# Kernel optimization log

Hardware: AMD Instinct MI355X
Metric: run time of the kernel (lower is better)

## Reference

```python
import jax, jax.numpy as jnp
import numpy as np

B, C, P = 16, 512, 4096


def setup_inputs() -> dict:
    key = jax.random.key(0)
    ks = jax.random.split(key, 7)
    s = 1.0 / np.sqrt(C)  # torch Conv1d default init scale
    return {
        "x": jax.random.normal(ks[0], (B, C, P), dtype=jnp.float32),
        "Wq": jax.random.uniform(ks[1], (C, C), jnp.float32, -s, s),
        "bq": jax.random.uniform(ks[2], (C,), jnp.float32, -s, s),
        "Wk": jax.random.uniform(ks[3], (C, C), jnp.float32, -s, s),
        "bk": jax.random.uniform(ks[4], (C,), jnp.float32, -s, s),
        "Wv": jax.random.uniform(ks[5], (C, C), jnp.float32, -s, s),
        "bv": jax.random.uniform(ks[6], (C,), jnp.float32, -s, s),
    }


def reference(x, Wq, bq, Wk, bk, Wv, bv):
    # 1x1 Conv1d == channel-mixing GEMM: out[b,o,p] = sum_i W[o,i] x[b,i,p] + b[o]
    q = jnp.einsum('oi,bip->bop', Wq, x) + bq[None, :, None]   # [B,C,P]
    k = jnp.einsum('oi,bip->bop', Wk, x) + bk[None, :, None]   # [B,C,P]
    v = jnp.einsum('oi,bip->bop', Wv, x) + bv[None, :, None]   # [B,C,P]
    energy = jnp.einsum('bcp,bdp->bcd', q, k)                  # [B,C,C] (unscaled)
    attn = jax.nn.softmax(energy, axis=-1)
    out = jnp.einsum('bcd,bdp->bcp', attn, v)                  # [B,C,P]
    return out
```

## Files before the change

### kernel.cpp

```cpp
#include <hip/hip_runtime.h>
#include <hip/hip_bf16.h>

#define CD 512
#define PD 4096
#define BD 16
#define CAUG 640
#define KW 576
#define GKS 4

typedef __bf16 bf16x8 __attribute__((ext_vector_type(8)));
typedef float f32x4 __attribute__((ext_vector_type(4)));
typedef unsigned short u16x8 __attribute__((ext_vector_type(8)));
typedef unsigned short u16x4 __attribute__((ext_vector_type(4)));

__device__ __forceinline__ unsigned short f2bf(float f) {
  unsigned u = __builtin_bit_cast(unsigned, f);
  u += 0x7FFFu + ((u >> 16) & 1u);
  return (unsigned short)(u >> 16);
}
__device__ __forceinline__ float bf2f(unsigned short h) {
  unsigned u = ((unsigned)h) << 16;
  return __builtin_bit_cast(float, u);
}

__global__ void convert_w2(const float* __restrict__ Wq, const float* __restrict__ bq,
                           const float* __restrict__ Wk, const float* __restrict__ bk,
                           const float* __restrict__ Wv,
                           unsigned short* __restrict__ Wqh, unsigned short* __restrict__ Wql,
                           unsigned short* __restrict__ Wkh, unsigned short* __restrict__ Wkl,
                           unsigned short* __restrict__ Wvh) {
  int i = blockIdx.x * 256 + threadIdx.x;
  if (i >= CD * KW) return;
  int o = i / KW, j = i - o * KW;
  float q = j < CD ? Wq[o * CD + j] : (j == CD ? bq[o] : 0.f);
  float k = j < CD ? Wk[o * CD + j] : (j == CD ? bk[o] : 0.f);
  unsigned short qh = f2bf(q), kh = f2bf(k);
  Wqh[i] = qh; Wql[i] = f2bf(q - bf2f(qh));
  Wkh[i] = kh; Wkl[i] = f2bf(k - bf2f(kh));
  if (j < CD) Wvh[o * CD + j] = f2bf(Wv[o * CD + j]);
}

__global__ void convert_x(const float* __restrict__ x, unsigned short* __restrict__ xsh,
                          unsigned short* __restrict__ xsl, unsigned short* __restrict__ xth) {
  int z = blockIdx.z, cy = blockIdx.y;
  int p0 = blockIdx.x * 64;
  int t = threadIdx.x;
  if (cy >= 8) {
    int row = 512 + (cy - 8) * 64 + (t >> 2);
    int cg = (t & 3) * 16;
    u16x8 h = (u16x8)0, l = (u16x8)0;
    if (row == 512)
#pragma unroll
      for (int i = 0; i < 8; ++i) h[i] = 0x3F80;
    size_t o = (size_t)z * CAUG * PD + (size_t)row * PD + p0 + cg;
    *reinterpret_cast<u16x8*>(xsh + o) = h;
    *reinterpret_cast<u16x8*>(xsh + o + 8) = h;
    *reinterpret_cast<u16x8*>(xsl + o) = l;
    *reinterpret_cast<u16x8*>(xsl + o + 8) = l;
    return;
  }
  __shared__ float tile[64][65];
  int c0 = cy * 64;
  const float* xb = x + (size_t)z * CD * PD;
  int tr = t >> 4, tc = t & 15;
#pragma unroll
  for (int j = 0; j < 4; ++j) {
    int r = tr + j * 16;
    const float* src = xb + (size_t)(c0 + r) * PD + p0 + tc * 4;
#pragma unroll
    for (int i = 0; i < 4; ++i) tile[r][tc * 4 + i] = src[i];
  }
  __syncthreads();
#pragma unroll
  for (int j = 0; j < 4; ++j) {
    int r = tr + j * 16;
    u16x4 hv, lv;
#pragma unroll
    for (int i = 0; i < 4; ++i) {
      float v = tile[r][tc * 4 + i];
      unsigned short h = f2bf(v);
      hv[i] = h; lv[i] = f2bf(v - bf2f(h));
    }
    size_t o = (size_t)z * CAUG * PD + (size_t)(c0 + r) * PD + p0 + tc * 4;
    *reinterpret_cast<u16x4*>(xsh + o) = hv;
    *reinterpret_cast<u16x4*>(xsl + o) = lv;
  }
#pragma unroll
  for (int j = 0; j < 4; ++j) {
    int pr = tr + j * 16;
    u16x4 hv;
#pragma unroll
    for (int i = 0; i < 4; ++i) hv[i] = f2bf(tile[tc * 4 + i][pr]);
    size_t o = (size_t)z * PD * CD + (size_t)(p0 + pr) * CD + c0 + tc * 4;
    *reinterpret_cast<u16x4*>(xth + o) = hv;
  }
}

enum { EPI_F32 = 0, EPI_HILO = 1, EPI_V = 2 };

template <int BM, int BN, int WM, int WN, bool SPLIT, int EPI, bool TRI, int SPLITK = 1>
__global__ __launch_bounds__((BM / WM) * (BN / WN) * 64) void gemm2(
    const unsigned short* __restrict__ Ahi, const unsigned short* __restrict__ Alo,
    const unsigned short* __restrict__ Bhi, const unsigned short* __restrict__ Blo,
    long long sA, long long sB, int ldA, int ldB, int K,
    float* __restrict__ Cf, unsigned short* __restrict__ Chi, unsigned short* __restrict__ Clo,
    long long sC, int ldC, const float* __restrict__ bias, int gx, int gy) {
  constexpr int BK = 64;
  constexpr int WAVES = (BM / WM) * (BN / WN);
  constexpr int NS = SPLIT ? 2 : 1;
  constexpr int MI = WM / 16, NI = WN / 16;
  constexpr int NWN = BN / WN;
  constexpr int CA = BM / 8, CB = BN / 8;
  constexpr int TOT = NS * (CA + CB);
  constexpr bool COMPACT = TRI && (SPLITK > 1);
  __shared__ unsigned short lds[NS * (BM + BN) * BK];

  int nwg = gridDim.x;
  int b = blockIdx.x;
  int q = nwg >> 3, r = nwg & 7, xcd = b & 7, pos = b >> 3;
  int wg = (xcd < r ? xcd * (q + 1) : r * (q + 1) + (xcd - r) * q) + pos;
  int bx, by, z, zc, tpi = 0, kbase = 0;
  if constexpr (TRI) {
    int tri = gy * (gy + 1) / 2;
    int perz = tri * SPLITK;
    z = wg / perz;
    int rem = wg - z * perz;
    int ks = rem / tri;
    tpi = rem - ks * tri;
    int tp = tpi;
    bx = 0;
    while (tp >= gy - bx) { tp -= gy - bx; ++bx; }
    by = bx + tp;
    kbase = ks * K;
    zc = z * SPLITK + ks;
  } else {
    by = wg % gy;
    int t2 = wg / gy;
    bx = t2 % gx;
    z = t2 / gx;
    zc = z;
  }

  const unsigned short* pA0 = Ahi + (size_t)z * sA + (size_t)bx * BM * ldA;
  const unsigned short* pB0 = Bhi + (size_t)z * sB + (size_t)by * BN * ldB;
  const unsigned short* pA1 = SPLIT ? Alo + (size_t)z * sA + (size_t)bx * BM * ldA : pA0;
  const unsigned short* pB1 = SPLIT ? Blo + (size_t)z * sB + (size_t)by * BN * ldB : pB0;

  int tid = threadIdx.x;
  int lane = tid & 63, wid = tid >> 6;
  int wr = wid / NWN, wc = wid % NWN;
  int lr = lane & 15, kh2 = lane >> 4;

  f32x4 acc[MI][NI] = {};

  for (int k0 = kbase; k0 < kbase + K; k0 += BK) {
#pragma unroll
    for (int i = 0; i < TOT / WAVES; ++i) {
      int c = wid + i * WAVES;
      const unsigned short* srcb; int ldX, lofs, rb2;
      if (c < CA)            { srcb = pA0; ldX = ldA; lofs = c * 512;                  rb2 = c * 8; }
      else if (c < NS * CA)  { srcb = pA1; ldX = ldA; lofs = BM * BK + (c - CA) * 512; rb2 = (c - CA) * 8; }
      else if (c < NS * CA + CB) { int cc = c - NS * CA; srcb = pB0; ldX = ldB;
                                   lofs = NS * BM * BK + cc * 512;                     rb2 = cc * 8; }
      else                   { int cc = c - NS * CA - CB; srcb = pB1; ldX = ldB;
                               lofs = NS * BM * BK + BN * BK + cc * 512;               rb2 = cc * 8; }
      int row = rb2 + (lane >> 3);
      const unsigned short* src =
          srcb + (size_t)row * ldX + k0 + (((lane & 7) ^ (row & 7)) << 3);
      __builtin_amdgcn_global_load_lds(
          (const __attribute__((address_space(1))) void*)src,
          (__attribute__((address_space(3))) void*)(lds + lofs), 16, 0, 0);
    }
    __syncthreads();

#pragma unroll
    for (int kk = 0; kk < BK / 32; ++kk) {
      bf16x8 ah[MI], al[MI], bh[NI], bl[NI];
#pragma unroll
      for (int m = 0; m < MI; ++m) {
        int row = wr * WM + m * 16 + lr;
        int so = ((((kk << 2) | kh2) ^ (row & 7)) << 3);
        ah[m] = *reinterpret_cast<const bf16x8*>(&lds[row * BK + so]);
        if constexpr (SPLIT)
          al[m] = *reinterpret_cast<const bf16x8*>(&lds[BM * BK + row * BK + so]);
      }
#pragma unroll
      for (int n = 0; n < NI; ++n) {
        int row = wc * WN + n * 16 + lr;
        int so = ((((kk << 2) | kh2) ^ (row & 7)) << 3);
        bh[n] = *reinterpret_cast<const bf16x8*>(&lds[NS * BM * BK + row * BK + so]);
        if constexpr (SPLIT)
          bl[n] = *reinterpret_cast<const bf16x8*>(&lds[NS * BM * BK + BN * BK + row * BK + so]);
      }
#pragma unroll
      for (int m = 0; m < MI; ++m)
#pragma unroll
        for (int n = 0; n < NI; ++n) {
          acc[m][n] = __builtin_amdgcn_mfma_f32_16x16x32_bf16(ah[m], bh[n], acc[m][n], 0, 0, 0);
          if constexpr (SPLIT) {
            acc[m][n] = __builtin_amdgcn_mfma_f32_16x16x32_bf16(ah[m], bl[n], acc[m][n], 0, 0, 0);
            acc[m][n] = __builtin_amdgcn_mfma_f32_16x16x32_bf16(al[m], bh[n], acc[m][n], 0, 0, 0);
          }
        }
    }
    __syncthreads();
  }

  int lg = lane >> 4;
#pragma unroll
  for (int m = 0; m < MI; ++m)
#pragma unroll
    for (int n = 0; n < NI; ++n) {
      int lcol = wc * WN + n * 16 + lr;
      float bcol = (EPI == EPI_V) ? bias[by * BN + lcol] : 0.f;
#pragma unroll
      for (int r4 = 0; r4 < 4; ++r4) {
        int lrow = wr * WM + m * 16 + lg * 4 + r4;
        float v = acc[m][n][r4];
        if constexpr (COMPACT) {
          size_t idx = (size_t)zc * sC + (size_t)tpi * (BM * BN) + (size_t)lrow * BN + lcol;
          Cf[idx] = v;
        } else {
          size_t idx = (size_t)zc * sC + (size_t)(bx * BM + lrow) * ldC + (by * BN + lcol);
          if constexpr (EPI == EPI_F32) {
            Cf[idx] = v;
          } else if constexpr (EPI == EPI_HILO) {
            unsigned short h = f2bf(v);
            Chi[idx] = h;
            Clo[idx] = f2bf(v - bf2f(h));
          } else {
            Chi[idx] = f2bf(v + bcol);
          }
        }
      }
    }
}

template <int KS>
__global__ void gram_reduce(const float* __restrict__ Gp,
                            unsigned short* __restrict__ Ghi, unsigned short* __restrict__ Glo) {
  int z = blockIdx.y;
  int tp = blockIdx.x;
  int b2 = tp, bx = 0;
  while (b2 >= 5 - bx) { b2 -= 5 - bx; ++bx; }
  int by = bx + b2;
  int t = threadIdx.x;
  const float* base = Gp + ((size_t)z * KS * 15 + tp) * (128 * 128);
  size_t gb = (size_t)z * CAUG * CAUG;
#pragma unroll
  for (int it = 0; it < 16; ++it) {
    int lrow = it * 8 + (t >> 5);
    int lc = (t & 31) * 4;
    f32x4 s = *reinterpret_cast<const f32x4*>(base + (size_t)lrow * 128 + lc);
#pragma unroll
    for (int ks = 1; ks < KS; ++ks)
      s += *reinterpret_cast<const f32x4*>(base + (size_t)ks * 15 * 128 * 128 +
                                           (size_t)lrow * 128 + lc);
    u16x4 h, l;
#pragma unroll
    for (int i = 0; i < 4; ++i) {
      unsigned short hh = f2bf(s[i]);
      h[i] = hh; l[i] = f2bf(s[i] - bf2f(hh));
    }
    size_t o = gb + (size_t)(bx * 128 + lrow) * CAUG + by * 128 + lc;
    *reinterpret_cast<u16x4*>(Ghi + o) = h;
    *reinterpret_cast<u16x4*>(Glo + o) = l;
  }
}

__global__ void mirror_g(unsigned short* __restrict__ Ghi, unsigned short* __restrict__ Glo) {
  __shared__ unsigned short shh[64][72], shl[64][72];
  int z = blockIdx.y;
  int pidx = blockIdx.x >> 2, sub = blockIdx.x & 3;
  int bx = 0, tp = pidx;
  while (tp >= 4 - bx) { tp -= 4 - bx; ++bx; }
  int by = bx + 1 + tp;
  int ti = bx * 2 + (sub & 1), tj = by * 2 + (sub >> 1);
  int t = threadIdx.x;
  int rr = t >> 2, cg = (t & 3) * 16;
  size_t gbase = (size_t)z * CAUG * CAUG;
  size_t so = gbase + (size_t)(ti * 64 + rr) * CAUG + tj * 64 + cg;
  *reinterpret_cast<u16x8*>(&shh[rr][cg]) = *reinterpret_cast<const u16x8*>(Ghi + so);
  *reinterpret_cast<u16x8*>(&shh[rr][cg + 8]) = *reinterpret_cast<const u16x8*>(Ghi + so + 8);
  *reinterpret_cast<u16x8*>(&shl[rr][cg]) = *reinterpret_cast<const u16x8*>(Glo + so);
  *reinterpret_cast<u16x8*>(&shl[rr][cg + 8]) = *reinterpret_cast<const u16x8*>(Glo + so + 8);
  __syncthreads();
  u16x8 oh, ol;
  size_t dst = gbase + (size_t)(tj * 64 + rr) * CAUG + ti * 64 + cg;
#pragma unroll
  for (int half = 0; half < 2; ++half) {
#pragma unroll
    for (int i = 0; i < 8; ++i) {
      oh[i] = shh[cg + half * 8 + i][rr];
      ol[i] = shl[cg + half * 8 + i][rr];
    }
    *reinterpret_cast<u16x8*>(Ghi + dst + half * 8) = oh;
    *reinterpret_cast<u16x8*>(Glo + dst + half * 8) = ol;
  }
}

__global__ void softmax_rows(const float* __restrict__ E, unsigned short* __restrict__ attn) {
  int lane = threadIdx.x & 63, wid = threadIdx.x >> 6;
  size_t row = (size_t)blockIdx.x * 4 + wid;
  const float* e = E + row * CD;
  const float4* ep = reinterpret_cast<const float4*>(e + lane * 8);
  float4 a = ep[0], bq4 = ep[1];
  float v[8] = {a.x, a.y, a.z, a.w, bq4.x, bq4.y, bq4.z, bq4.w};
  float m = v[0];
#pragma unroll
  for (int i = 1; i < 8; ++i) m = fmaxf(m, v[i]);
  for (int o = 32; o > 0; o >>= 1) m = fmaxf(m, __shfl_xor(m, o));
  float s = 0.f;
#pragma unroll
  for (int i = 0; i < 8; ++i) { v[i] = __expf(v[i] - m); s += v[i]; }
  for (int o = 32; o > 0; o >>= 1) s += __shfl_xor(s, o);
  float rinv = 1.0f / s;
  u16x4 h0, h1;
#pragma unroll
  for (int i = 0; i < 4; ++i) { h0[i] = f2bf(v[i] * rinv); h1[i] = f2bf(v[4 + i] * rinv); }
  unsigned short* op = attn + row * CD + lane * 8;
  *reinterpret_cast<u16x4*>(op) = h0;
  *reinterpret_cast<u16x4*>(op + 4) = h1;
}

extern "C" void kernel_launch(void* const* d_in, const int* in_sizes, int n_in,
                              void* d_out, int out_size, void* d_ws, size_t ws_size,
                              hipStream_t stream) {
  (void)in_sizes; (void)n_in; (void)out_size;
  const float* x  = (const float*)d_in[0];
  const float* Wq = (const float*)d_in[1];
  const float* bq = (const float*)d_in[2];
  const float* Wk = (const float*)d_in[3];
  const float* bk = (const float*)d_in[4];
  const float* Wv = (const float*)d_in[5];
  const float* bv = (const float*)d_in[6];
  float* out = (float*)d_out;

  char* base = (char*)d_ws;
  size_t off = 0;
  auto carve = [&](size_t bytes) -> char* {
    char* p = base + off;
    off += (bytes + 255) & ~(size_t)255;
    return p;
  };
  unsigned short* Wqh = (unsigned short*)carve((size_t)CD * KW * 2);
  unsigned short* Wql = (unsigned short*)carve((size_t)CD * KW * 2);
  unsigned short* Wkh = (unsigned short*)carve((size_t)CD * KW * 2);
  unsigned short* Wkl = (unsigned short*)carve((size_t)CD * KW * 2);
  unsigned short* Wvh = (unsigned short*)carve((size_t)CD * CD * 2);

  const size_t CP = (size_t)CD * PD;
  const size_t XS = (size_t)CAUG * PD;
  const size_t XT = (size_t)PD * CD;
  const size_t GG = (size_t)CAUG * CAUG;
  const size_t TT = (size_t)CD * CAUG;
  const size_t EE = (size_t)CD * CD;
  const size_t per_batch = 2 * XS * 2 + XT * 2 + 2 * GG * 2 + 2 * TT * 2 + EE * 4 + EE * 2 + XT * 2 + 2048;
  size_t rem = (ws_size > off + 4096) ? (ws_size - off - 4096) : 0;
  int nb = (int)(rem / per_batch);
  if (nb < 1) nb = 1;
  if (nb > BD) nb = BD;

  unsigned short* xsh = (unsigned short*)carve((size_t)nb * XS * 2);
  unsigned short* xsl = (unsigned short*)carve((size_t)nb * XS * 2);
  unsigned short* xth = (unsigned short*)carve((size_t)nb * XT * 2);
  unsigned short* Ghi = (unsigned short*)carve((size_t)nb * GG * 2);
  unsigned short* Glo = (unsigned short*)carve((size_t)nb * GG * 2);
  unsigned short* Thi = (unsigned short*)carve((size_t)nb * TT * 2);
  unsigned short* Tlo = (unsigned short*)carve((size_t)nb * TT * 2);
  float*          E   = (float*)carve((size_t)nb * EE * 4);
  unsigned short* att = (unsigned short*)carve((size_t)nb * EE * 2);
  unsigned short* vT  = (unsigned short*)carve((size_t)nb * XT * 2);

  float* Gpart = E;

  convert_w2<<<dim3((CD * KW + 255) / 256), 256, 0, stream>>>(
      Wq, bq, Wk, bk, Wv, Wqh, Wql, Wkh, Wkl, Wvh);

  for (int b0 = 0; b0 < BD; b0 += nb) {
    int cb = (BD - b0 < nb) ? (BD - b0) : nb;

    convert_x<<<dim3(PD / 64, 10, cb), 256, 0, stream>>>(x + (size_t)b0 * CP, xsh, xsl, xth);

    gemm2<128, 128, 64, 32, true, EPI_F32, true, GKS><<<15 * GKS * cb, 512, 0, stream>>>(
        xsh, xsl, xsh, xsl, (long long)XS, (long long)XS, PD, PD, PD / GKS,
        Gpart, nullptr, nullptr, (long long)15 * 128 * 128, 128, nullptr, 5, 5);

    gram_reduce<GKS><<<dim3(15, cb), 256, 0, stream>>>(Gpart, Ghi, Glo);

    mirror_g<<<dim3(40, cb), 256, 0, stream>>>(Ghi, Glo);

    gemm2<64, 64, 32, 32, true, EPI_HILO, false><<<8 * 10 * cb, 256, 0, stream>>>(
        Wqh, Wql, Ghi, Glo, 0, (long long)GG, KW, CAUG, KW,
        nullptr, Thi, Tlo, (long long)TT, CAUG, nullptr, 8, 10);

    gemm2<64, 64, 32, 32, true, EPI_F32, false><<<8 * 8 * cb, 256, 0, stream>>>(
        Thi, Tlo, Wkh, Wkl, (long long)TT, 0, CAUG, KW, KW,
        E, nullptr, nullptr, (long long)EE, CD, nullptr, 8, 8);

    softmax_rows<<<dim3(cb * CD / 4), 256, 0, stream>>>(E, att);

    gemm2<128, 128, 64, 64, false, EPI_V, false><<<32 * 4 * cb, 256, 0, stream>>>(
        xth, nullptr, Wvh, nullptr, (long long)XT, 0, CD, CD, CD,
        nullptr, vT, nullptr, (long long)XT, CD, bv, 32, 4);

    gemm2<128, 128, 64, 64, false, EPI_F32, false><<<4 * 32 * cb, 256, 0, stream>>>(
        att, nullptr, vT, nullptr, (long long)EE, (long long)XT, CD, CD, CD,
        out + (size_t)b0 * CP, nullptr, nullptr, (long long)CP, PD, nullptr, 4, 32);
  }
}
```

Before: 352.6 us.

## Drop bias-augmented Gram; apply bias terms as rank-one corrections in softmax

Instead of augmenting x with a ones row and padding the channel dimension to 640/576, the Gram matrix and the Wq·G·Wk^T chain now run on the exact 512 channels. Bias contributions are computed separately: convert_x produces per-channel row sums of x, a small kernel forms u = Wq·r + P·bq and w = Wk·r, and softmax adds u_c·bk_d + bq_c·w_d (the bq·bk constant is dropped since it cancels in softmax). This removes roughly a third of the Gram GEMM work and the padded downstream GEMM sizes, at the cost of a serial per-batch uvw kernel and extra loads in softmax. Gram split-K also rises from 4 to 8.

Measured after the change: 400.3 us. 1.14x slower.

```diff
diff --git a/kernel.cpp b/kernel.cpp
--- a/kernel.cpp
+++ b/kernel.cpp
@@ -4,9 +4,8 @@
 #define CD 512
 #define PD 4096
 #define BD 16
-#define CAUG 640
-#define KW 576
-#define GKS 4
+#define GKS 8
+#define NTRI 10
 
 typedef __bf16 bf16x8 __attribute__((ext_vector_type(8)));
 typedef float f32x4 __attribute__((ext_vector_type(4)));
@@ -23,45 +22,28 @@
   return __builtin_bit_cast(float, u);
 }
 
-__global__ void convert_w2(const float* __restrict__ Wq, const float* __restrict__ bq,
-                           const float* __restrict__ Wk, const float* __restrict__ bk,
+__global__ void convert_w2(const float* __restrict__ Wq, const float* __restrict__ Wk,
                            const float* __restrict__ Wv,
                            unsigned short* __restrict__ Wqh, unsigned short* __restrict__ Wql,
                            unsigned short* __restrict__ Wkh, unsigned short* __restrict__ Wkl,
                            unsigned short* __restrict__ Wvh) {
   int i = blockIdx.x * 256 + threadIdx.x;
-  if (i >= CD * KW) return;
-  int o = i / KW, j = i - o * KW;
-  float q = j < CD ? Wq[o * CD + j] : (j == CD ? bq[o] : 0.f);
-  float k = j < CD ? Wk[o * CD + j] : (j == CD ? bk[o] : 0.f);
-  unsigned short qh = f2bf(q), kh = f2bf(k);
+  if (i >= CD * CD) return;
+  float q = Wq[i]; unsigned short qh = f2bf(q);
   Wqh[i] = qh; Wql[i] = f2bf(q - bf2f(qh));
+  float k = Wk[i]; unsigned short kh = f2bf(k);
   Wkh[i] = kh; Wkl[i] = f2bf(k - bf2f(kh));
-  if (j < CD) Wvh[o * CD + j] = f2bf(Wv[o * CD + j]);
+  Wvh[i] = f2bf(Wv[i]);
 }
 
 __global__ void convert_x(const float* __restrict__ x, unsigned short* __restrict__ xsh,
-                          unsigned short* __restrict__ xsl, unsigned short* __restrict__ xth) {
-  int z = blockIdx.z, cy = blockIdx.y;
-  int p0 = blockIdx.x * 64;
+                          unsigned short* __restrict__ xsl, unsigned short* __restrict__ xth,
+                          float* __restrict__ r_part) {
+  __shared__ float tile[64][65];
+  int z = blockIdx.z;
+  int c0 = blockIdx.y * 64, p0 = blockIdx.x * 64;
+  const float* xb = x + (size_t)z * CD * PD;
   int t = threadIdx.x;
-  if (cy >= 8) {
-    int row = 512 + (cy - 8) * 64 + (t >> 2);
-    int cg = (t & 3) * 16;
-    u16x8 h = (u16x8)0, l = (u16x8)0;
-    if (row == 512)
-#pragma unroll
-      for (int i = 0; i < 8; ++i) h[i] = 0x3F80;
-    size_t o = (size_t)z * CAUG * PD + (size_t)row * PD + p0 + cg;
-    *reinterpret_cast<u16x8*>(xsh + o) = h;
-    *reinterpret_cast<u16x8*>(xsh + o + 8) = h;
-    *reinterpret_cast<u16x8*>(xsl + o) = l;
-    *reinterpret_cast<u16x8*>(xsl + o + 8) = l;
-    return;
-  }
-  __shared__ float tile[64][65];
-  int c0 = cy * 64;
-  const float* xb = x + (size_t)z * CD * PD;
   int tr = t >> 4, tc = t & 15;
 #pragma unroll
   for (int j = 0; j < 4; ++j) {
@@ -81,7 +63,7 @@
       unsigned short h = f2bf(v);
       hv[i] = h; lv[i] = f2bf(v - bf2f(h));
     }
-    size_t o = (size_t)z * CAUG * PD + (size_t)(c0 + r) * PD + p0 + tc * 4;
+    size_t o = (size_t)z * CD * PD + (size_t)(c0 + r) * PD + p0 + tc * 4;
     *reinterpret_cast<u16x4*>(xsh + o) = hv;
     *reinterpret_cast<u16x4*>(xsl + o) = lv;
   }
@@ -94,6 +76,36 @@
     size_t o = (size_t)z * PD * CD + (size_t)(p0 + pr) * CD + c0 + tc * 4;
     *reinterpret_cast<u16x4*>(xth + o) = hv;
   }
+  {
+    int row = t >> 2, q4 = t & 3;
+    float s = 0.f;
+#pragma unroll
+    for (int i = 0; i < 16; ++i) s += tile[row][q4 * 16 + i];
+    s += __shfl_xor(s, 1);
+    s += __shfl_xor(s, 2);
+    if (q4 == 0)
+      r_part[((size_t)z * CD + c0 + row) * 64 + (p0 >> 6)] = s;
+  }
+}
+
+__global__ void uvw_kernel(const float* __restrict__ r_part, const float* __restrict__ Wq,
+                           const float* __restrict__ bq, const float* __restrict__ Wk,
+                           float* __restrict__ uw) {
+  __shared__ float rl[CD];
+  int z = blockIdx.x;
+  int c = threadIdx.x;
+  const float* rp = r_part + ((size_t)z * CD + c) * 64;
+  float s = 0.f;
+#pragma unroll
+  for (int pb = 0; pb < 64; ++pb) s += rp[pb];
+  rl[c] = s;
+  __syncthreads();
+  float du = 0.f, dw = 0.f;
+  const float* wq = Wq + (size_t)c * CD;
+  const float* wk = Wk + (size_t)c * CD;
+  for (int i = 0; i < CD; ++i) { du += wq[i] * rl[i]; dw += wk[i] * rl[i]; }
+  uw[(size_t)z * 2 * CD + c] = du + (float)PD * bq[c];
+  uw[(size_t)z * 2 * CD + CD + c] = dw;
 }
 
 enum { EPI_F32 = 0, EPI_HILO = 1, EPI_V = 2 };
@@ -242,11 +254,11 @@
   int z = blockIdx.y;
   int tp = blockIdx.x;
   int b2 = tp, bx = 0;
-  while (b2 >= 5 - bx) { b2 -= 5 - bx; ++bx; }
+  while (b2 >= 4 - bx) { b2 -= 4 - bx; ++bx; }
   int by = bx + b2;
   int t = threadIdx.x;
-  const float* base = Gp + ((size_t)z * KS * 15 + tp) * (128 * 128);
-  size_t gb = (size_t)z * CAUG * CAUG;
+  const float* base = Gp + ((size_t)z * KS * NTRI + tp) * (128 * 128);
+  size_t gb = (size_t)z * CD * CD;
 #pragma unroll
   for (int it = 0; it < 16; ++it) {
     int lrow = it * 8 + (t >> 5);
@@ -254,7 +266,7 @@
     f32x4 s = *reinterpret_cast<const f32x4*>(base + (size_t)lrow * 128 + lc);
 #pragma unroll
     for (int ks = 1; ks < KS; ++ks)
-      s += *reinterpret_cast<const f32x4*>(base + (size_t)ks * 15 * 128 * 128 +
+      s += *reinterpret_cast<const f32x4*>(base + (size_t)ks * NTRI * 128 * 128 +
                                            (size_t)lrow * 128 + lc);
     u16x4 h, l;
 #pragma unroll
@@ -262,7 +274,7 @@
       unsigned short hh = f2bf(s[i]);
       h[i] = hh; l[i] = f2bf(s[i] - bf2f(hh));
     }
-    size_t o = gb + (size_t)(bx * 128 + lrow) * CAUG + by * 128 + lc;
+    size_t o = gb + (size_t)(bx * 128 + lrow) * CD + by * 128 + lc;
     *reinterpret_cast<u16x4*>(Ghi + o) = h;
     *reinterpret_cast<u16x4*>(Glo + o) = l;
   }
@@ -273,20 +285,20 @@
   int z = blockIdx.y;
   int pidx = blockIdx.x >> 2, sub = blockIdx.x & 3;
   int bx = 0, tp = pidx;
-  while (tp >= 4 - bx) { tp -= 4 - bx; ++bx; }
+  while (tp >= 3 - bx) { tp -= 3 - bx; ++bx; }
   int by = bx + 1 + tp;
   int ti = bx * 2 + (sub & 1), tj = by * 2 + (sub >> 1);
   int t = threadIdx.x;
   int rr = t >> 2, cg = (t & 3) * 16;
-  size_t gbase = (size_t)z * CAUG * CAUG;
-  size_t so = gbase + (size_t)(ti * 64 + rr) * CAUG + tj * 64 + cg;
+  size_t gbase = (size_t)z * CD * CD;
+  size_t so = gbase + (size_t)(ti * 64 + rr) * CD + tj * 64 + cg;
   *reinterpret_cast<u16x8*>(&shh[rr][cg]) = *reinterpret_cast<const u16x8*>(Ghi + so);
   *reinterpret_cast<u16x8*>(&shh[rr][cg + 8]) = *reinterpret_cast<const u16x8*>(Ghi + so + 8);
   *reinterpret_cast<u16x8*>(&shl[rr][cg]) = *reinterpret_cast<const u16x8*>(Glo + so);
   *reinterpret_cast<u16x8*>(&shl[rr][cg + 8]) = *reinterpret_cast<const u16x8*>(Glo + so + 8);
   __syncthreads();
   u16x8 oh, ol;
-  size_t dst = gbase + (size_t)(tj * 64 + rr) * CAUG + ti * 64 + cg;
+  size_t dst = gbase + (size_t)(tj * 64 + rr) * CD + ti * 64 + cg;
 #pragma unroll
   for (int half = 0; half < 2; ++half) {
 #pragma unroll
@@ -299,13 +311,27 @@
   }
 }
 
-__global__ void softmax_rows(const float* __restrict__ E, unsigned short* __restrict__ attn) {
+__global__ void softmax_rows(const float* __restrict__ E, unsigned short* __restrict__ attn,
+                             const float* __restrict__ bq, const float* __restrict__ bk,
+                             const float* __restrict__ uw) {
   int lane = threadIdx.x & 63, wid = threadIdx.x >> 6;
   size_t row = (size_t)blockIdx.x * 4 + wid;
+  int z = (int)(row >> 9), c = (int)(row & 511);
+  float uc = uw[(size_t)z * 2 * CD + c];
+  float bqc = bq[c];
+  const float* wp = uw + (size_t)z * 2 * CD + CD;
   const float* e = E + row * CD;
-  const float4* ep = reinterpret_cast<const float4*>(e + lane * 8);
-  float4 a = ep[0], bq4 = ep[1];
-  float v[8] = {a.x, a.y, a.z, a.w, bq4.x, bq4.y, bq4.z, bq4.w};
+  int d0 = lane * 8;
+  const float4* ep = reinterpret_cast<const float4*>(e + d0);
+  float4 a = ep[0], b4 = ep[1];
+  float4 k0 = *reinterpret_cast<const float4*>(bk + d0);
+  float4 k1 = *reinterpret_cast<const float4*>(bk + d0 + 4);
+  float4 w0 = *reinterpret_cast<const float4*>(wp + d0);
+  float4 w1 = *reinterpret_cast<const float4*>(wp + d0 + 4);
+  float v[8] = {a.x + uc * k0.x + bqc * w0.x, a.y + uc * k0.y + bqc * w0.y,
+                a.z + uc * k0.z + bqc * w0.z, a.w + uc * k0.w + bqc * w0.w,
+                b4.x + uc * k1.x + bqc * w1.x, b4.y + uc * k1.y + bqc * w1.y,
+                b4.z + uc * k1.z + bqc * w1.z, b4.w + uc * k1.w + bqc * w1.w};
   float m = v[0];
 #pragma unroll
   for (int i = 1; i < 8; ++i) m = fmaxf(m, v[i]);
@@ -318,7 +344,7 @@
   u16x4 h0, h1;
 #pragma unroll
   for (int i = 0; i < 4; ++i) { h0[i] = f2bf(v[i] * rinv); h1[i] = f2bf(v[4 + i] * rinv); }
-  unsigned short* op = attn + row * CD + lane * 8;
+  unsigned short* op = attn + row * CD + d0;
   *reinterpret_cast<u16x4*>(op) = h0;
   *reinterpret_cast<u16x4*>(op + 4) = h1;
 }
@@ -343,69 +369,73 @@
     off += (bytes + 255) & ~(size_t)255;
     return p;
   };
-  unsigned short* Wqh = (unsigned short*)carve((size_t)CD * KW * 2);
-  unsigned short* Wql = (unsigned short*)carve((size_t)CD * KW * 2);
-  unsigned short* Wkh = (unsigned short*)carve((size_t)CD * KW * 2);
-  unsigned short* Wkl = (unsigned short*)carve((size_t)CD * KW * 2);
-  unsigned short* Wvh = (unsigned short*)carve((size_t)CD * CD * 2);
+  const size_t WB = (size_t)CD * CD * 2;
+  unsigned short* Wqh = (unsigned short*)carve(WB);
+  unsigned short* Wql = (unsigned short*)carve(WB);
+  unsigned short* Wkh = (unsigned short*)carve(WB);
+  unsigned short* Wkl = (unsigned short*)carve(WB);
+  unsigned short* Wvh = (unsigned short*)carve(WB);
 
   const size_t CP = (size_t)CD * PD;
-  const size_t XS = (size_t)CAUG * PD;
-  const size_t XT = (size_t)PD * CD;
-  const size_t GG = (size_t)CAUG * CAUG;
-  const size_t TT = (size_t)CD * CAUG;
+  const size_t GG = (size_t)CD * CD;
   const size_t EE = (size_t)CD * CD;
-  const size_t per_batch = 2 * XS * 2 + XT * 2 + 2 * GG * 2 + 2 * TT * 2 + EE * 4 + EE * 2 + XT * 2 + 2048;
+  const size_t per_batch = 3 * CP * 2 + 4 * GG * 2 + (size_t)CD * 64 * 4 + 2 * CD * 4 +
+                           EE * 4 + EE * 2 + CP * 2 + 4096;
   size_t rem = (ws_size > off + 4096) ? (ws_size - off - 4096) : 0;
   int nb = (int)(rem / per_batch);
   if (nb < 1) nb = 1;
   if (nb > BD) nb = BD;
 
-  unsigned short* xsh = (unsigned short*)carve((size_t)nb * XS * 2);
-  unsigned short* xsl = (unsigned short*)carve((size_t)nb * XS * 2);
-  unsigned short* xth = (unsigned short*)carve((size_t)nb * XT * 2);
+  unsigned short* xsh = (unsigned short*)carve((size_t)nb * CP * 2);
+  unsigned short* xsl = (unsigned short*)carve((size_t)nb * CP * 2);
+  unsigned short* xth = (unsigned short*)carve((size_t)nb * CP * 2);
   unsigned short* Ghi = (unsigned short*)carve((size_t)nb * GG * 2);
   unsigned short* Glo = (unsigned short*)carve((size_t)nb * GG * 2);
-  unsigned short* Thi = (unsigned short*)carve((size_t)nb * TT * 2);
-  unsigned short* Tlo = (unsigned short*)carve((size_t)nb * TT * 2);
+  unsigned short* Thi = (unsigned short*)carve((size_t)nb * GG * 2);
+  unsigned short* Tlo = (unsigned short*)carve((size_t)nb * GG * 2);
+  float*          r_part = (float*)carve((size_t)nb * CD * 64 * 4);
+  float*          uw  = (float*)carve((size_t)nb * 2 * CD * 4);
   float*          E   = (float*)carve((size_t)nb * EE * 4);
   unsigned short* att = (unsigned short*)carve((size_t)nb * EE * 2);
-  unsigned short* vT  = (unsigned short*)carve((size_t)nb * XT * 2);
+  unsigned short* vT  = (unsigned short*)carve((size_t)nb * CP * 2);
 
   float* Gpart = E;
 
-  convert_w2<<<dim3((CD * KW + 255) / 256), 256, 0, stream>>>(
-      Wq, bq, Wk, bk, Wv, Wqh, Wql, Wkh, Wkl, Wvh);
+  convert_w2<<<dim3((CD * CD + 255) / 256), 256, 0, stream>>>(
+      Wq, Wk, Wv, Wqh, Wql, Wkh, Wkl, Wvh);
 
   for (int b0 = 0; b0 < BD; b0 += nb) {
     int cb = (BD - b0 < nb) ? (BD - b0) : nb;
 
-    convert_x<<<dim3(PD / 64, 10, cb), 256, 0, stream>>>(x + (size_t)b0 * CP, xsh, xsl, xth);
-
-    gemm2<128, 128, 64, 32, true, EPI_F32, true, GKS><<<15 * GKS * cb, 512, 0, stream>>>(
-        xsh, xsl, xsh, xsl, (long long)XS, (long long)XS, PD, PD, PD / GKS,
-        Gpart, nullptr, nullptr, (long long)15 * 128 * 128, 128, nullptr, 5, 5);
-
-    gram_reduce<GKS><<<dim3(15, cb), 256, 0, stream>>>(Gpart, Ghi, Glo);
-
-    mirror_g<<<dim3(40, cb), 256, 0, stream>>>(Ghi, Glo);
-
-    gemm2<64, 64, 32, 32, true, EPI_HILO, false><<<8 * 10 * cb, 256, 0, stream>>>(
-        Wqh, Wql, Ghi, Glo, 0, (long long)GG, KW, CAUG, KW,
-        nullptr, Thi, Tlo, (long long)TT, CAUG, nullptr, 8, 10);
+    convert_x<<<dim3(PD / 64, CD / 64, cb), 256, 0, stream>>>(
+        x + (size_t)b0 * CP, xsh, xsl, xth, r_part);
+
+    uvw_kernel<<<dim3(cb), 512, 0, stream>>>(r_part, Wq, bq, Wk, uw);
+
+    gemm2<128, 128, 64, 32, true, EPI_F32, true, GKS><<<NTRI * GKS * cb, 512, 0, stream>>>(
+        xsh, xsl, xsh, xsl, (long long)CP, (long long)CP, PD, PD, PD / GKS,
+        Gpart, nullptr, nullptr, (long long)NTRI * 128 * 128, 128, nullptr, 4, 4);
+
+    gram_reduce<GKS><<<dim3(NTRI, cb), 256, 0, stream>>>(Gpart, Ghi, Glo);
+
+    mirror_g<<<dim3(24, cb), 256, 0, stream>>>(Ghi, Glo);
+
+    gemm2<64, 64, 32, 32, true, EPI_HILO, false><<<8 * 8 * cb, 256, 0, stream>>>(
+        Wqh, Wql, Ghi, Glo, 0, (long long)GG, CD, CD, CD,
+        nullptr, Thi, Tlo, (long long)GG, CD, nullptr, 8, 8);
 
     gemm2<64, 64, 32, 32, true, EPI_F32, false><<<8 * 8 * cb, 256, 0, stream>>>(
-        Thi, Tlo, Wkh, Wkl, (long long)TT, 0, CAUG, KW, KW,
+        Thi, Tlo, Wkh, Wkl, (long long)GG, 0, CD, CD, CD,
         E, nullptr, nullptr, (long long)EE, CD, nullptr, 8, 8);
 
-    softmax_rows<<<dim3(cb * CD / 4), 256, 0, stream>>>(E, att);
+    softmax_rows<<<dim3(cb * CD / 4), 256, 0, stream>>>(E, att, bq, bk, uw);
 
     gemm2<128, 128, 64, 64, false, EPI_V, false><<<32 * 4 * cb, 256, 0, stream>>>(
-        xth, nullptr, Wvh, nullptr, (long long)XT, 0, CD, CD, CD,
-        nullptr, vT, nullptr, (long long)XT, CD, bv, 32, 4);
+        xth, nullptr, Wvh, nullptr, (long long)CP, 0, CD, CD, CD,
+        nullptr, vT, nullptr, (long long)CP, CD, bv, 32, 4);
 
     gemm2<128, 128, 64, 64, false, EPI_F32, false><<<4 * 32 * cb, 256, 0, stream>>>(
-        att, nullptr, vT, nullptr, (long long)EE, (long long)XT, CD, CD, CD,
+        att, nullptr, vT, nullptr, (long long)EE, (long long)CP, CD, CD, CD,
         out + (size_t)b0 * CP, nullptr, nullptr, (long long)CP, PD, nullptr, 4, 32);
   }
 }
```
